# Kernel tuning notes

Measured on AMD Instinct MI355X. Metric: run time of the kernel, lower is better.

## Reference

```python
import jax, jax.numpy as jnp
import numpy as np

N, C, T, V = 16, 128, 150, 25
NH, DK, DV = 8, 32, 128          # dk = 0.25*128, dv = out_channels
DKH, DVH = DK // NH, DV // NH    # 4, 16
EPS = 1e-5


def setup_inputs() -> dict:
    key = jax.random.key(0)
    ks = jax.random.split(key, 14)
    qkv_out = 2 * DK + DV  # 192
    return {
        "x": jax.random.normal(ks[0], (N, C, T, V), jnp.float32),
        "qkv_w": jax.random.normal(ks[1], (qkv_out, C), jnp.float32) * (1.0 / np.sqrt(C)),
        "qkv_b": jax.random.normal(ks[2], (qkv_out,), jnp.float32) * 0.01,
        "key_rel": jax.random.normal(ks[3], (2 * T - 1, DKH), jnp.float32),
        "attn_w": jax.random.normal(ks[4], (DV, DV), jnp.float32) * (1.0 / np.sqrt(DV)),
        "attn_b": jax.random.normal(ks[5], (DV,), jnp.float32) * 0.01,
        "dbn_g": jnp.ones((C * V,), jnp.float32),
        "dbn_b": jnp.zeros((C * V,), jnp.float32),
        "dbn_m": jax.random.normal(ks[6], (C * V,), jnp.float32) * 0.01,
        "dbn_v": jax.random.uniform(ks[7], (C * V,), jnp.float32, 0.5, 1.5),
        "bn_g": jnp.ones((DV,), jnp.float32),
        "bn_b": jnp.zeros((DV,), jnp.float32),
        "bn_m": jax.random.normal(ks[8], (DV,), jnp.float32) * 0.01,
        "bn_v": jax.random.uniform(ks[9], (DV,), jnp.float32, 0.5, 1.5),
    }


def rel_to_abs(x):
    # x: [B, H, L, 2L-1] relative logits -> [B, H, L, L] absolute logits
    B, H, L, _ = x.shape
    x = jnp.pad(x, ((0, 0), (0, 0), (0, 0), (0, 1)))          # [B,H,L,2L]
    flat = x.reshape(B, H, L * 2 * L)
    flat = jnp.pad(flat, ((0, 0), (0, 0), (0, L - 1)))
    return flat.reshape(B, H, L + 1, 2 * L - 1)[:, :, :L, L - 1:]


def reference(x, qkv_w, qkv_b, key_rel, attn_w, attn_b,
              dbn_g, dbn_b, dbn_m, dbn_v, bn_g, bn_b, bn_m, bn_v):
    n, c, t, v = x.shape
    x_sum = x
    # data_bn (BatchNorm1d over C*V channels, inference mode)
    xn = x.transpose(0, 1, 3, 2).reshape(n, c * v, t)
    xn = (xn - dbn_m[None, :, None]) * (dbn_g / jnp.sqrt(dbn_v + EPS))[None, :, None] + dbn_b[None, :, None]
    xn = xn.reshape(n, c, v, t).transpose(0, 1, 3, 2)
    # fold nodes into batch: [N,C,T,V] -> [N*V, C, T]
    xb = xn.transpose(0, 3, 1, 2).reshape(n * v, c, t)
    # pointwise qkv conv (kernel 1x1)
    qkv = jnp.einsum('bct,oc->bot', xb, qkv_w) + qkv_b[None, :, None]
    q = qkv[:, :DK]
    k = qkv[:, DK:2 * DK]
    val = qkv[:, 2 * DK:]
    B = n * v
    q = q.reshape(B, NH, DKH, t) * (DKH ** -0.5)   # scaled before rel logits, as in torch
    k = k.reshape(B, NH, DKH, t)
    val = val.reshape(B, NH, DVH, t)
    logits = jnp.einsum('bhdt,bhds->bhts', q, k)    # [B,NH,T,T]
    rel = jnp.einsum('bhdt,md->bhtm', q, key_rel)   # [B,NH,T,2T-1]
    logits = logits + rel_to_abs(rel)
    weights = jax.nn.softmax(logits, axis=-1)
    out = jnp.einsum('bhts,bhds->bhtd', weights, val)  # [B,NH,T,DVH]
    # combine heads -> [B, DV, T], then 1x1 attn_out conv
    out = out.transpose(0, 1, 3, 2).reshape(B, DV, t)
    out = jnp.einsum('bct,oc->bot', out, attn_w) + attn_b[None, :, None]
    # unfold nodes: [N*V, DV, T] -> [N, DV, T, V]
    out = out.reshape(n, v, DV, t).transpose(0, 2, 3, 1)
    res = out + x_sum
    # BatchNorm2d over channel dim (inference mode)
    res = (res - bn_m[None, :, None, None]) * (bn_g / jnp.sqrt(bn_v + EPS))[None, :, None, None] + bn_b[None, :, None, None]
    return jax.nn.relu(res)
```

## Files before the change

kernel.cpp:

```cpp
#include <hip/hip_runtime.h>
#include <math.h>

#define N_   16
#define C_   128
#define T_   150
#define V_   25
#define NH_  8
#define DK_  32
#define DV_  128
#define B_   400
#define QO_  192
#define EPS_ 1e-5f

typedef __attribute__((ext_vector_type(4))) short bf16x4;
typedef __attribute__((ext_vector_type(4))) float f32x4;
typedef __attribute__((ext_vector_type(8))) short short8;

__device__ inline f32x4 mfma16(bf16x4 a, bf16x4 b, f32x4 c) {
#if __has_builtin(__builtin_amdgcn_mfma_f32_16x16x16bf16_1k)
  return __builtin_amdgcn_mfma_f32_16x16x16bf16_1k(a, b, c, 0, 0, 0);
#else
  asm volatile("v_mfma_f32_16x16x16_bf16 %0, %1, %2, %0"
               : "+v"(c) : "v"(a), "v"(b));
  return c;
#endif
}

__device__ inline short f2bf(float f) {
  union { float f; unsigned u; } v; v.f = f;
  unsigned u = v.u + 0x7fffu + ((v.u >> 16) & 1u);
  return (short)(u >> 16);
}
__device__ inline float lo16(unsigned u) { union { unsigned u; float f; } v; v.u = u << 16;        return v.f; }
__device__ inline float hi16(unsigned u) { union { unsigned u; float f; } v; v.u = u & 0xffff0000u; return v.f; }
__device__ inline unsigned pk2(float a, float b) {
  union { float f; unsigned u; } x, y; x.f = a; y.f = b;
  return ((x.u + 0x8000u) >> 16) | ((y.u + 0x8000u) & 0xffff0000u);
}

__global__ __launch_bounds__(256) void k_prep(
    const float* __restrict__ qkv_w, const float* __restrict__ attn_w,
    const float* __restrict__ dbn_g, const float* __restrict__ dbn_b,
    const float* __restrict__ dbn_m, const float* __restrict__ dbn_v,
    short* __restrict__ wqb, short* __restrict__ wab,
    float* __restrict__ dsc, float* __restrict__ dsh)
{
  const int tid = blockIdx.x*256 + threadIdx.x;
  const int nthr = gridDim.x*256;
  for (int i = tid; i < QO_*C_; i += nthr) wqb[i] = f2bf(qkv_w[i]);
  for (int i = tid; i < DV_*DV_; i += nthr) wab[i] = f2bf(attn_w[i]);
  for (int i = tid; i < C_*V_; i += nthr) {
    float sc = dbn_g[i] * rsqrtf(dbn_v[i] + EPS_);
    dsc[i] = sc;
    dsh[i] = dbn_b[i] - dbn_m[i]*sc;
  }
}

__global__ __launch_bounds__(256) void k_xt2(
    const float* __restrict__ x, const float* __restrict__ dsc,
    const float* __restrict__ dsh, short* __restrict__ xtb)
{
  const int n = blockIdx.x, tv0 = blockIdx.y * 125;
  __shared__ short ls[C_][126];
  for (int i = threadIdx.x; i < C_*125; i += 256) {
    int c = i / 125, j = i % 125;
    int cv = c*V_ + j % 25;
    ls[c][j] = f2bf(x[((size_t)n*C_ + c)*(T_*V_) + tv0 + j] * dsc[cv] + dsh[cv]);
  }
  __syncthreads();
  for (int i = threadIdx.x; i < 125*C_; i += 256) {
    int j = i >> 7, c = i & 127;
    int tv = tv0 + j, t = tv / 25, v = tv % 25;
    xtb[((size_t)(n*V_ + v)*T_ + t)*C_ + c] = ls[c][j];
  }
}

__global__ __launch_bounds__(256) void k_qkv(
    const short* __restrict__ xtb, const short* __restrict__ wqb,
    const float* __restrict__ qkv_b, short* __restrict__ qkvb)
{
  const int b = blockIdx.x, t0 = blockIdx.y * 80;
  __shared__ short xs[80][136];
  for (int i = threadIdx.x; i < 80*16; i += 256) {
    int tt = i >> 4, ch = i & 15, t = t0 + tt;
    short8 vv = {0,0,0,0,0,0,0,0};
    if (t < T_) vv = *(const short8*)&xtb[((size_t)b*T_ + t)*C_ + ch*8];
    *(short8*)&xs[tt][ch*8] = vv;
  }
  __syncthreads();
  const int wave = threadIdx.x >> 6, lane = threadIdx.x & 63;
  const int tl = lane & 15, g = lane >> 4;
  const int ob = wave * 48;

  bf16x4 afr[3][8];
  #pragma unroll
  for (int mt = 0; mt < 3; ++mt)
    #pragma unroll
    for (int ks = 0; ks < 8; ++ks)
      afr[mt][ks] = *(const bf16x4*)&wqb[(ob + mt*16 + tl)*C_ + ks*16 + g*4];

  const f32x4 zero = {0.f,0.f,0.f,0.f};
  f32x4 acc[3][5];
  #pragma unroll
  for (int mt = 0; mt < 3; ++mt)
    #pragma unroll
    for (int nt = 0; nt < 5; ++nt) acc[mt][nt] = zero;

  #pragma unroll
  for (int ks = 0; ks < 8; ++ks) {
    bf16x4 bfr[5];
    #pragma unroll
    for (int nt = 0; nt < 5; ++nt)
      bfr[nt] = *(const bf16x4*)&xs[nt*16 + tl][ks*16 + g*4];
    #pragma unroll
    for (int mt = 0; mt < 3; ++mt)
      #pragma unroll
      for (int nt = 0; nt < 5; ++nt)
        acc[mt][nt] = mfma16(afr[mt][ks], bfr[nt], acc[mt][nt]);
  }

  float bia[3][4];
  #pragma unroll
  for (int mt = 0; mt < 3; ++mt)
    #pragma unroll
    for (int r = 0; r < 4; ++r) bia[mt][r] = qkv_b[ob + mt*16 + g*4 + r];

  #pragma unroll
  for (int nt = 0; nt < 5; ++nt) {
    int tg = t0 + nt*16 + tl;
    if (tg >= T_) continue;
    #pragma unroll
    for (int mt = 0; mt < 3; ++mt) {
      int o = ob + mt*16 + g*4;
      short* dst = &qkvb[((size_t)b*QO_ + o)*T_ + tg];
      #pragma unroll
      for (int r = 0; r < 4; ++r)
        dst[r*T_] = f2bf(acc[mt][nt][r] + bia[mt][r]);
    }
  }
}

__global__ __launch_bounds__(256) void k_attn(
    const short* __restrict__ qkvb, const float* __restrict__ key_rel,
    short* __restrict__ o2b)
{
  const int bh = blockIdx.x;
  const int b  = bh >> 3, h = bh & 7;
  __shared__ short kb[160][20];
  __shared__ short qb[160][20];
  __shared__ short ve[16][164];
  __shared__ float relf[328][4];
  const short* base = qkvb + (size_t)b*QO_*T_;
  const int tid = threadIdx.x;
  const float QSC = 0.5f * 1.44269504f;

  for (int i = tid; i < 4*160; i += 256) {
    int d = i / 160, s = i % 160;
    kb[s][d] = (s < T_) ? base[(DK_ + h*4 + d)*T_ + s] : (short)0;
  }
  for (int i = tid; i < 4*160; i += 256) {
    int d = i / 160, t = i % 160;
    short qv = (t < T_) ? base[(h*4 + d)*T_ + t] : (short)0;
    union { unsigned u; float f; } uf; uf.u = ((unsigned)(unsigned short)qv) << 16;
    qb[t][d] = f2bf(uf.f * QSC);
  }
  for (int i = tid; i < 160*12; i += 256) {
    int s = i / 12, j = i % 12 + 4;
    kb[s][j] = 0; qb[s][j] = 0;
  }
  for (int i = tid; i < 16*160; i += 256) {
    int e = i / 160, s = i % 160;
    ve[e][s] = (s < T_) ? base[(2*DK_ + h*16 + e)*T_ + s] : (short)0;
  }
  for (int i = tid; i < 328*4; i += 256) {
    int m4 = i - 64;
    relf[i >> 2][i & 3] = (m4 >= 0 && m4 < (2*T_-1)*4) ? key_rel[m4] : 0.f;
  }
  __syncthreads();

  const int wave = tid >> 6, lane = tid & 63;
  const int tl = lane & 15, soff = (lane >> 4) << 2;

  bf16x4 kfr[10], vfr[10];
  #pragma unroll
  for (int st = 0; st < 10; ++st) {
    kfr[st] = *(const bf16x4*)&kb[st*16 + tl][soff];
    vfr[st] = *(const bf16x4*)&ve[tl][st*16 + soff];
  }

  const f32x4 zero = {0.f, 0.f, 0.f, 0.f};

  for (int tt = wave; tt < 10; tt += 4) {
    const int t0 = tt*16, tg = t0 + tl;
    const bf16x4 qfr = *(const bf16x4*)&qb[tg][soff];
    f32x4 c[10];
    #pragma unroll
    for (int st = 0; st < 10; ++st) c[st] = mfma16(kfr[st], qfr, zero);

    unsigned qv0 = *(const unsigned*)&qb[tg][0];
    unsigned qv1 = *(const unsigned*)&qb[tg][2];
    const float q0 = lo16(qv0), q1 = hi16(qv0), q2 = lo16(qv1), q3 = hi16(qv1);

    const float* rb = &relf[soff - tl - t0 + 149 + 16][0];
    #pragma unroll
    for (int st = 0; st < 10; ++st) {
      #pragma unroll
      for (int i = 0; i < 4; ++i) {
        float4 rv = *(const float4*)(rb + (st*16 + i)*4);
        c[st][i] = fmaf(q0, rv.x, fmaf(q1, rv.y, fmaf(q2, rv.z,
                   fmaf(q3, rv.w, c[st][i]))));
      }
    }
    #pragma unroll
    for (int i = 0; i < 4; ++i)
      if (soff + i >= 6) c[9][i] = -3.0e38f;

    float l = 0.f;
    f32x4 acc = zero;
    #pragma unroll
    for (int st = 0; st < 10; ++st) {
      float p0 = __builtin_exp2f(c[st][0]);
      float p1 = __builtin_exp2f(c[st][1]);
      float p2 = __builtin_exp2f(c[st][2]);
      float p3 = __builtin_exp2f(c[st][3]);
      l += (p0 + p1) + (p2 + p3);
      union { unsigned u[2]; bf16x4 v; } pf;
      pf.u[0] = pk2(p0, p1); pf.u[1] = pk2(p2, p3);
      acc = mfma16(vfr[st], pf.v, acc);
    }
    l += __shfl_xor(l, 16);
    l += __shfl_xor(l, 32);
    const float inv = __builtin_amdgcn_rcpf(l);

    if (tg < T_) {
      unsigned u0 = pk2(acc[0]*inv, acc[1]*inv);
      unsigned u1 = pk2(acc[2]*inv, acc[3]*inv);
      *(uint2*)&o2b[((size_t)b*T_ + tg)*DV_ + h*16 + soff] = make_uint2(u0, u1);
    }
  }
}

__global__ __launch_bounds__(256) void k_proj(
    const short* __restrict__ o2b, const short* __restrict__ wab,
    const float* __restrict__ attn_b, short* __restrict__ projb)
{
  const int b = blockIdx.x, t0 = blockIdx.y * 80;
  __shared__ short xs[80][136];
  for (int i = threadIdx.x; i < 80*16; i += 256) {
    int tt = i >> 4, ch = i & 15, t = t0 + tt;
    short8 vv = {0,0,0,0,0,0,0,0};
    if (t < T_) vv = *(const short8*)&o2b[((size_t)b*T_ + t)*DV_ + ch*8];
    *(short8*)&xs[tt][ch*8] = vv;
  }
  __syncthreads();
  const int wave = threadIdx.x >> 6, lane = threadIdx.x & 63;
  const int tl = lane & 15, g = lane >> 4;
  const int ob = wave * 32;

  bf16x4 afr[2][8];
  #pragma unroll
  for (int mt = 0; mt < 2; ++mt)
    #pragma unroll
    for (int ks = 0; ks < 8; ++ks)
      afr[mt][ks] = *(const bf16x4*)&wab[(ob + mt*16 + tl)*DV_ + ks*16 + g*4];

  const f32x4 zero = {0.f,0.f,0.f,0.f};
  f32x4 acc[2][5];
  #pragma unroll
  for (int mt = 0; mt < 2; ++mt)
    #pragma unroll
    for (int nt = 0; nt < 5; ++nt) acc[mt][nt] = zero;

  #pragma unroll
  for (int ks = 0; ks < 8; ++ks) {
    bf16x4 bfr[5];
    #pragma unroll
    for (int nt = 0; nt < 5; ++nt)
      bfr[nt] = *(const bf16x4*)&xs[nt*16 + tl][ks*16 + g*4];
    #pragma unroll
    for (int mt = 0; mt < 2; ++mt)
      #pragma unroll
      for (int nt = 0; nt < 5; ++nt)
        acc[mt][nt] = mfma16(afr[mt][ks], bfr[nt], acc[mt][nt]);
  }

  float bia[2][4];
  #pragma unroll
  for (int mt = 0; mt < 2; ++mt)
    #pragma unroll
    for (int r = 0; r < 4; ++r) bia[mt][r] = attn_b[ob + mt*16 + g*4 + r];

  #pragma unroll
  for (int nt = 0; nt < 5; ++nt) {
    int tg = t0 + nt*16 + tl;
    if (tg >= T_) continue;
    #pragma unroll
    for (int mt = 0; mt < 2; ++mt) {
      int o = ob + mt*16 + g*4;
      short* dst = &projb[((size_t)b*DV_ + o)*T_ + tg];
      #pragma unroll
      for (int r = 0; r < 4; ++r)
        dst[r*T_] = f2bf(acc[mt][nt][r] + bia[mt][r]);
    }
  }
}

__global__ __launch_bounds__(256) void k_final(
    const short* __restrict__ projb, const float* __restrict__ x,
    const float* __restrict__ bn_g, const float* __restrict__ bn_b,
    const float* __restrict__ bn_m, const float* __restrict__ bn_v,
    float* __restrict__ out)
{
  const int n = blockIdx.x, o = blockIdx.y;
  __shared__ short ls[V_*T_];
  for (int i = threadIdx.x; i < V_*T_; i += 256) {
    int v = i / T_, t = i % T_;
    ls[i] = projb[((size_t)(n*V_ + v)*DV_ + o)*T_ + t];
  }
  __syncthreads();
  const float sc = bn_g[o] * rsqrtf(bn_v[o] + EPS_);
  const float sh = bn_b[o] - bn_m[o]*sc;
  const size_t base = ((size_t)n*C_ + o)*(T_*V_);
  for (int j = threadIdx.x; j < T_*V_; j += 256) {
    int t = j / V_, v = j % V_;
    float pv = lo16((unsigned)(unsigned short)ls[v*T_ + t]);
    float r = (pv + x[base + j]) * sc + sh;
    out[base + j] = fmaxf(r, 0.f);
  }
}

extern "C" void kernel_launch(void* const* d_in, const int* in_sizes, int n_in,
                              void* d_out, int out_size, void* d_ws, size_t ws_size,
                              hipStream_t stream) {
  const float* x       = (const float*)d_in[0];
  const float* qkv_w   = (const float*)d_in[1];
  const float* qkv_b   = (const float*)d_in[2];
  const float* key_rel = (const float*)d_in[3];
  const float* attn_w  = (const float*)d_in[4];
  const float* attn_b  = (const float*)d_in[5];
  const float* dbn_g   = (const float*)d_in[6];
  const float* dbn_b   = (const float*)d_in[7];
  const float* dbn_m   = (const float*)d_in[8];
  const float* dbn_v   = (const float*)d_in[9];
  const float* bn_g    = (const float*)d_in[10];
  const float* bn_b    = (const float*)d_in[11];
  const float* bn_m    = (const float*)d_in[12];
  const float* bn_v    = (const float*)d_in[13];

  short* xtb  = (short*)d_ws;
  short* o2b  = xtb;
  short* qkvb = xtb + (size_t)B_*C_*T_;
  float* projf = (float*)(qkvb + (size_t)B_*QO_*T_);
  short* projb = (short*)projf;
  float* dsc  = projf + (size_t)B_*DV_*T_;
  float* dsh  = dsc + C_*V_;
  short* wqb  = (short*)(dsh + C_*V_);
  short* wab  = wqb + QO_*C_;
  float* outp = (float*)d_out;

  k_prep<<<32, 256, 0, stream>>>(qkv_w, attn_w, dbn_g, dbn_b, dbn_m, dbn_v,
                                 wqb, wab, dsc, dsh);
  k_xt2<<<dim3(N_, 30), 256, 0, stream>>>(x, dsc, dsh, xtb);
  k_qkv<<<dim3(B_, 2), 256, 0, stream>>>(xtb, wqb, qkv_b, qkvb);
  k_attn<<<dim3(B_*NH_), 256, 0, stream>>>(qkvb, key_rel, o2b);
  k_proj<<<dim3(B_, 2), 256, 0, stream>>>(o2b, wab, attn_b, projb);
  k_final<<<dim3(N_, DV_), 256, 0, stream>>>(projb, x, bn_g, bn_b, bn_m, bn_v, outp);
}
```

Baseline: 142.5 us.

## Compute relative-position logits with MFMA via block-diagonal Q instead of FMAs

Replaces the per-lane scalar FMA loop that added q·key_rel relative logits with MFMA instructions. key_rel is stored in shared memory as bf16, and Q is spread into four sparse B fragments so that each MFMA adds the rel_to_abs shifted dot products directly into the logit accumulators. This moves 160 FMAs per lane onto the matrix cores at the cost of 40 extra MFMAs per tile, mostly multiplying zeros. It also lowers the rel term precision to bf16 key_rel.

```diff
diff --git a/kernel.cpp b/kernel.cpp
--- a/kernel.cpp
+++ b/kernel.cpp
@@ -149,7 +149,7 @@
   __shared__ short kb[160][20];
   __shared__ short qb[160][20];
   __shared__ short ve[16][164];
-  __shared__ float relf[328][4];
+  __shared__ short krb[336*4];
   const short* base = qkvb + (size_t)b*QO_*T_;
   const int tid = threadIdx.x;
   const float QSC = 0.5f * 1.44269504f;
@@ -172,14 +172,14 @@
     int e = i / 160, s = i % 160;
     ve[e][s] = (s < T_) ? base[(2*DK_ + h*16 + e)*T_ + s] : (short)0;
   }
-  for (int i = tid; i < 328*4; i += 256) {
-    int m4 = i - 64;
-    relf[i >> 2][i & 3] = (m4 >= 0 && m4 < (2*T_-1)*4) ? key_rel[m4] : 0.f;
+  for (int i = tid; i < 336*4; i += 256) {
+    int m = (i >> 2) - 16;
+    krb[i] = (m >= 0 && m < 2*T_-1) ? f2bf(key_rel[m*4 + (i & 3)]) : (short)0;
   }
   __syncthreads();
 
   const int wave = tid >> 6, lane = tid & 63;
-  const int tl = lane & 15, soff = (lane >> 4) << 2;
+  const int tl = lane & 15, g = lane >> 4, soff = g << 2;
 
   bf16x4 kfr[10], vfr[10];
   #pragma unroll
@@ -189,6 +189,9 @@
   }
 
   const f32x4 zero = {0.f, 0.f, 0.f, 0.f};
+  const bf16x4 zerob = {0, 0, 0, 0};
+  const bool act = (g == (tl & 3));
+  const int kca = tl >> 2;
 
   for (int tt = wave; tt < 10; tt += 4) {
     const int t0 = tt*16, tg = t0 + tl;
@@ -197,20 +200,21 @@
     #pragma unroll
     for (int st = 0; st < 10; ++st) c[st] = mfma16(kfr[st], qfr, zero);
 
-    unsigned qv0 = *(const unsigned*)&qb[tg][0];
-    unsigned qv1 = *(const unsigned*)&qb[tg][2];
-    const float q0 = lo16(qv0), q1 = hi16(qv0), q2 = lo16(qv1), q3 = hi16(qv1);
-
-    const float* rb = &relf[soff - tl - t0 + 149 + 16][0];
-    #pragma unroll
-    for (int st = 0; st < 10; ++st) {
-      #pragma unroll
-      for (int i = 0; i < 4; ++i) {
-        float4 rv = *(const float4*)(rb + (st*16 + i)*4);
-        c[st][i] = fmaf(q0, rv.x, fmaf(q1, rv.y, fmaf(q2, rv.z,
-                   fmaf(q3, rv.w, c[st][i]))));
-      }
-    }
+    union { unsigned u[2]; bf16x4 v; } bqu;
+    bqu.u[0] = *(const unsigned*)&qb[tg][0];
+    bqu.u[1] = *(const unsigned*)&qb[tg][2];
+    bf16x4 brel[4];
+    #pragma unroll
+    for (int kc = 0; kc < 4; ++kc)
+      brel[kc] = (act && kc == kca) ? bqu.v : zerob;
+
+    const bf16x4* krp = ((const bf16x4*)krb) + (tl - g + 165 - t0);
+    #pragma unroll
+    for (int st = 0; st < 10; ++st)
+      #pragma unroll
+      for (int kc = 0; kc < 4; ++kc)
+        c[st] = mfma16(krp[st*16 - kc*4], brel[kc], c[st]);
+
     #pragma unroll
     for (int i = 0; i < 4; ++i)
       if (soff + i >= 6) c[9][i] = -3.0e38f;
```

After: 140.1 us. About the same (-1.7%).
